# Kernel optimization log

Measured on AMD Instinct MI355X. Metric: run time of the kernel, lower is better.

## Reference

```python
import jax, jax.numpy as jnp
import numpy as np
import math

EMBED_DIM = 64
NUM_HEADS = 4
HEAD_DIM = EMBED_DIM // NUM_HEADS
TGT = 64
SRC = 64
BSZ = 128


def setup_inputs() -> dict:
    key = jax.random.key(0)
    ks = jax.random.split(key, 8)
    x = jax.random.normal(ks[0], (TGT, BSZ, EMBED_DIM), dtype=jnp.float32)
    relation = jax.random.normal(ks[1], (TGT, SRC, BSZ, EMBED_DIM), dtype=jnp.float32)
    in_proj_weight = jax.random.normal(ks[2], (3 * EMBED_DIM, EMBED_DIM), dtype=jnp.float32) * 0.02
    in_proj_bias = jnp.zeros((3 * EMBED_DIM,), dtype=jnp.float32)
    rel_weight = jax.random.normal(ks[3], (2 * EMBED_DIM, EMBED_DIM), dtype=jnp.float32) * 0.02
    rel_bias = jnp.zeros((2 * EMBED_DIM,), dtype=jnp.float32)
    out_weight = jax.random.normal(ks[4], (EMBED_DIM, EMBED_DIM), dtype=jnp.float32) * 0.02
    out_bias = jnp.zeros((EMBED_DIM,), dtype=jnp.float32)
    return {
        'query': x, 'key': x, 'value': x, 'relation': relation,
        'in_proj_weight': in_proj_weight, 'in_proj_bias': in_proj_bias,
        'rel_weight': rel_weight, 'rel_bias': rel_bias,
        'out_weight': out_weight, 'out_bias': out_bias,
    }


def reference(query, key, value, relation, in_proj_weight, in_proj_bias,
              rel_weight, rel_bias, out_weight, out_bias):
    E, H, hd = EMBED_DIM, NUM_HEADS, HEAD_DIM
    t, b, _ = query.shape
    s = key.shape[0]
    scaling = hd ** (-0.5)
    # qkv projections (slices of the fused in_proj weight, as in _in_proj)
    q = query @ in_proj_weight[:E].T + in_proj_bias[:E]
    k = key @ in_proj_weight[E:2 * E].T + in_proj_bias[E:2 * E]
    v = value @ in_proj_weight[2 * E:].T + in_proj_bias[2 * E:]
    q = q.reshape(t, b * H, hd)
    k = k.reshape(s, b * H, hd)
    v = v.reshape(s, b * H, hd)
    # relation projection -> ra, rb, each [t, s, b*H, hd], then transpose(0,1)
    rel = relation @ rel_weight.T + rel_bias  # [t, s, b, 2E]
    ra = rel[..., :E].reshape(t, s, b * H, hd).swapaxes(0, 1)  # [s, t, bH, hd]
    rb = rel[..., E:].reshape(t, s, b * H, hd).swapaxes(0, 1)
    # q[i,j] = q[i] + ra_t[i,j]; requires t == s (broadcast as in torch)
    qp = (q[:, None] + ra) * scaling            # [t, s, bH, hd]
    kp = k[None, :] + rb                        # [t, s, bH, hd]
    attn_weights = jnp.einsum('ijbn,ijbn->ijb', qp, kp) * (1.0 / math.sqrt(hd))
    attn_weights = jax.nn.softmax(attn_weights, axis=1)
    attn = jnp.einsum('ijb,jbn->bin', attn_weights, v)  # [bH, t, hd]
    attn = attn.swapaxes(0, 1).reshape(t, b, E)
    out = attn @ out_weight.T + out_bias
    return out
```

## Files before the change

kernel.cpp:

```cpp
#include <hip/hip_runtime.h>
#include <hip/hip_bf16.h>

#define T_ 64
#define S_ 64
#define B_ 128
#define E_ 64
#define H_ 4

typedef float f32x4 __attribute__((ext_vector_type(4)));
typedef short bf16x8 __attribute__((ext_vector_type(8)));

static __device__ __forceinline__ short f2b(float f) {
    union { __hip_bfloat16 h; short s; } u;
    u.h = __float2bfloat16(f);
    return u.s;
}

__global__ __launch_bounds__(256) void k_qkv(
    const float* __restrict__ qin, const float* __restrict__ kin,
    const float* __restrict__ vin, const float* __restrict__ W,
    const float* __restrict__ bias, float* __restrict__ qkv,
    const float* __restrict__ relW, const float* __restrict__ relBias,
    ushort* __restrict__ wBf, unsigned int* __restrict__ kpbW)
{
    const int tid = threadIdx.x;

    if (blockIdx.x == 256) {
        #pragma unroll
        for (int li = 0; li < 8; ++li) {
            int f4 = li * 256 + tid;
            int o = f4 >> 4, e4 = f4 & 15;
            float4 wv = reinterpret_cast<const float4*>(relW)[f4];
            ushort4 bv;
            bv.x = (ushort)f2b(wv.x); bv.y = (ushort)f2b(wv.y);
            bv.z = (ushort)f2b(wv.z); bv.w = (ushort)f2b(wv.w);
            int ot = o >> 4, cc = o & 15;
            int ks = e4 >> 3, rqb = (e4 & 7) >> 1, half = e4 & 1;
            int dest = (ot * 2 + ks) * 512 + (rqb * 16 + cc) * 8 + half * 4;
            *reinterpret_cast<ushort4*>(wBf + dest) = bv;
        }
        #pragma unroll
        for (int li = 0; li < 8; ++li) {
            int t = li * 256 + tid;
            int ot = t >> 9, lane = (t >> 3) & 63, e = t & 7;
            int cI = lane & 15, rqI = lane >> 4;
            wBf[8192 + t] =
                (rqI * 8 + e == (ot & 1) * 16 + cI) ? (ushort)0x3F80 : (ushort)0;
        }
        return;
    }

    __shared__ float xs[3][32 * 68];
    __shared__ float WTs[64 * 68];
    const int row0 = blockIdx.x * 32;

    #pragma unroll
    for (int l = 0; l < 6; ++l) {
        int f4 = l * 256 + tid;
        int src = f4 >> 9, rem = f4 & 511;
        int r = rem >> 4, e0 = (rem & 15) << 2;
        const float* xin = (src == 0) ? qin : (src == 1 ? kin : vin);
        float4 xv = reinterpret_cast<const float4*>(xin)[(size_t)(row0 + r) * 16 + (e0 >> 2)];
        float* dst = &xs[src][r * 68];
        dst[e0] = xv.x; dst[e0 + 1] = xv.y; dst[e0 + 2] = xv.z; dst[e0 + 3] = xv.w;
    }

    const int rq = tid >> 5, og = tid & 31;
    const int r0 = rq * 4, op0 = og * 2;

    for (int seg = 0; seg < 3; ++seg) {
        __syncthreads();
        #pragma unroll
        for (int l = 0; l < 4; ++l) {
            int f4 = l * 256 + tid;
            int o = f4 >> 4, e0 = (f4 & 15) << 2;
            float4 wv = reinterpret_cast<const float4*>(W)[(size_t)(seg * 64 + o) * 16 + (e0 >> 2)];
            WTs[(e0 + 0) * 68 + o] = wv.x; WTs[(e0 + 1) * 68 + o] = wv.y;
            WTs[(e0 + 2) * 68 + o] = wv.z; WTs[(e0 + 3) * 68 + o] = wv.w;
        }
        __syncthreads();

        float acc[4][2];
        #pragma unroll
        for (int rr = 0; rr < 4; ++rr) {
            acc[rr][0] = bias[seg * 64 + op0];
            acc[rr][1] = bias[seg * 64 + op0 + 1];
        }
        const float* xsrc = xs[seg];
        #pragma unroll 4
        for (int e = 0; e < 64; ++e) {
            float w0 = WTs[e * 68 + op0];
            float w1 = WTs[e * 68 + op0 + 1];
            #pragma unroll
            for (int rr = 0; rr < 4; ++rr) {
                float xv = xsrc[(r0 + rr) * 68 + e];
                acc[rr][0] += xv * w0;
                acc[rr][1] += xv * w1;
            }
        }
        #pragma unroll
        for (int rr = 0; rr < 4; ++rr) {
            float2 ov = make_float2(acc[rr][0], acc[rr][1]);
            reinterpret_cast<float2*>(
                &qkv[((size_t)seg * T_ * B_ + row0 + r0 + rr) * E_ + op0])[0] = ov;
        }
        if (seg == 1) {
            #pragma unroll
            for (int rr = 0; rr < 4; ++rr) {
                int row = row0 + r0 + rr;
                int jj = row >> 7, b = row & 127;
                float kb0 = acc[rr][0] + relBias[64 + op0];
                float kb1 = acc[rr][1] + relBias[64 + op0 + 1];
                unsigned int u = (unsigned int)(ushort)f2b(kb0) |
                                 ((unsigned int)(ushort)f2b(kb1) << 16);
                int off = jj * 8192 + (op0 >> 5) * 4096 + (b >> 4) * 512 +
                          ((b & 15) + ((op0 & 31) >> 3) * 16) * 8 + (op0 & 7);
                kpbW[off >> 1] = u;
            }
        }
    }
}

__global__ __launch_bounds__(512, 4) void k_logits_mfma(
    const float* __restrict__ rel, const ushort* __restrict__ wBf,
    const ushort* __restrict__ kpbF, const float* __restrict__ relBias,
    const float* __restrict__ qkv, float* __restrict__ logits)
{
    __shared__ char  Bs[20480];
    __shared__ float llds[8][64][9];

    const int tid = threadIdx.x;
    const int w = tid >> 6, l = tid & 63;
    const int c = l & 15, rq = l >> 4;
    const int i = blockIdx.x >> 3;
    const int jb = (blockIdx.x & 7) * 8;

    #pragma unroll
    for (int li = 0; li < 3; ++li) {
        int idx = li * 512 + tid;
        if (idx < 1280)
            reinterpret_cast<float4*>(Bs)[idx] =
                reinterpret_cast<const float4*>(wBf)[idx];
    }

    float qpre[4][4];
    {
        const float* qrow = qkv + (size_t)i * (B_ * E_);
        #pragma unroll
        for (int h = 0; h < 4; ++h) {
            float ba = relBias[h * 16 + c];
            #pragma unroll
            for (int r = 0; r < 4; ++r)
                qpre[h][r] = qrow[(w * 16 + rq * 4 + r) * E_ + h * 16 + c] + ba;
        }
    }
    __syncthreads();

    const int arow = (w * 16 + c) * E_ + rq * 8;
    const int kfo  = w * 512 + l * 8;

    float4 x0, x1, x2, x3;
    {
        const float* ab = rel + ((size_t)jb * S_ + i) * (size_t)(B_ * E_) + arow;
        x0 = *(const float4*)(ab);
        x1 = *(const float4*)(ab + 4);
        x2 = *(const float4*)(ab + 32);
        x3 = *(const float4*)(ab + 36);
    }

    #pragma unroll 1
    for (int t = 0; t < 8; ++t) {
        const int j = jb + t;

        bf16x8 kf0 = *(const bf16x8*)(kpbF + (size_t)j * 8192 + kfo);
        bf16x8 kf1 = *(const bf16x8*)(kpbF + (size_t)j * 8192 + 4096 + kfo);

        bf16x8 af0, af1;
        {
            bf16x8 a;
            a[0] = f2b(x0.x); a[1] = f2b(x0.y); a[2] = f2b(x0.z); a[3] = f2b(x0.w);
            a[4] = f2b(x1.x); a[5] = f2b(x1.y); a[6] = f2b(x1.z); a[7] = f2b(x1.w);
            af0 = a;
            a[0] = f2b(x2.x); a[1] = f2b(x2.y); a[2] = f2b(x2.z); a[3] = f2b(x2.w);
            a[4] = f2b(x3.x); a[5] = f2b(x3.y); a[6] = f2b(x3.z); a[7] = f2b(x3.w);
            af1 = a;
        }

        if (t < 7) {
            const float* ab = rel + ((size_t)(j + 1) * S_ + i) * (size_t)(B_ * E_) + arow;
            x0 = *(const float4*)(ab);
            x1 = *(const float4*)(ab + 4);
            x2 = *(const float4*)(ab + 32);
            x3 = *(const float4*)(ab + 36);
        }

        int bs0 = 0;
        asm volatile("" : "+v"(bs0));
        const char* bsp = Bs + bs0;

        f32x4 acc[8];
        #pragma unroll
        for (int ot = 0; ot < 8; ++ot) acc[ot] = (f32x4){0.f, 0.f, 0.f, 0.f};
        #pragma unroll
        for (int ot = 0; ot < 4; ++ot) {
            acc[ot] = __builtin_amdgcn_mfma_f32_16x16x32_bf16(
                af0, *(const bf16x8*)(bsp + (ot * 2 + 0) * 1024 + l * 16), acc[ot], 0, 0, 0);
            acc[ot] = __builtin_amdgcn_mfma_f32_16x16x32_bf16(
                af1, *(const bf16x8*)(bsp + (ot * 2 + 1) * 1024 + l * 16), acc[ot], 0, 0, 0);
        }
        #pragma unroll
        for (int ot = 0; ot < 4; ++ot) {
            acc[4 + ot] = __builtin_amdgcn_mfma_f32_16x16x32_bf16(
                af0, *(const bf16x8*)(bsp + (8 + ot * 2 + 0) * 1024 + l * 16), acc[4 + ot], 0, 0, 0);
            acc[4 + ot] = __builtin_amdgcn_mfma_f32_16x16x32_bf16(
                af1, *(const bf16x8*)(bsp + (8 + ot * 2 + 1) * 1024 + l * 16), acc[4 + ot], 0, 0, 0);
            acc[4 + ot] = __builtin_amdgcn_mfma_f32_16x16x32_bf16(
                (ot < 2 ? kf0 : kf1),
                *(const bf16x8*)(bsp + (16 + ot) * 1024 + l * 16), acc[4 + ot], 0, 0, 0);
        }

        float v[16];
        #pragma unroll
        for (int h = 0; h < 4; ++h)
            #pragma unroll
            for (int r = 0; r < 4; ++r)
                v[h * 4 + r] = (qpre[h][r] + acc[h][r]) * acc[4 + h][r];
        #pragma unroll
        for (int k = 0; k < 8; ++k) {
            float x = (c & 1) ? v[2 * k + 1] : v[2 * k];
            float y = (c & 1) ? v[2 * k] : v[2 * k + 1];
            v[k] = x + __shfl_xor(y, 1);
        }
        #pragma unroll
        for (int k = 0; k < 4; ++k) {
            float x = (c & 2) ? v[2 * k + 1] : v[2 * k];
            float y = (c & 2) ? v[2 * k] : v[2 * k + 1];
            v[k] = x + __shfl_xor(y, 2);
        }
        #pragma unroll
        for (int k = 0; k < 2; ++k) {
            float x = (c & 4) ? v[2 * k + 1] : v[2 * k];
            float y = (c & 4) ? v[2 * k] : v[2 * k + 1];
            v[k] = x + __shfl_xor(y, 4);
        }
        {
            float x = (c & 8) ? v[1] : v[0];
            float y = (c & 8) ? v[0] : v[1];
            llds[w][l][t] = (x + __shfl_xor(y, 8)) * 0.0625f;
        }
    }

    {
        float f[8];
        #pragma unroll
        for (int t2 = 0; t2 < 8; ++t2) f[t2] = llds[w][l][t2];
        const int hh = c >> 2, rr = c & 3;
        const int b = w * 16 + rq * 4 + rr;
        float* dst = &logits[(((size_t)i * B_ + b) * H_ + hh) * S_ + jb];
        *reinterpret_cast<float4*>(dst) = make_float4(f[0], f[1], f[2], f[3]);
        *reinterpret_cast<float4*>(dst + 4) = make_float4(f[4], f[5], f[6], f[7]);
    }
}

__global__ __launch_bounds__(256) void k_attn(
    const float* __restrict__ logits, const float* __restrict__ qkv,
    const float* __restrict__ Wout, const float* __restrict__ bout,
    float* __restrict__ out)
{
    __shared__ float wsm[4][H_][S_];
    __shared__ float ap[4][68];
    const int tid = threadIdx.x;
    const int i = blockIdx.x >> 5;
    const int bq = blockIdx.x & 31;
    const int w = tid >> 6, l = tid & 63;
    const int b = bq * 4 + w;

    const float* lg = logits + ((size_t)i * B_ + b) * H_ * S_;
    const int h = l >> 4, sub = l & 15;
    float v0 = lg[h * S_ + sub];
    float v1 = lg[h * S_ + sub + 16];
    float v2 = lg[h * S_ + sub + 32];
    float v3 = lg[h * S_ + sub + 48];
    float m = fmaxf(fmaxf(v0, v1), fmaxf(v2, v3));
    #pragma unroll
    for (int d = 1; d < 16; d <<= 1) m = fmaxf(m, __shfl_xor(m, d));
    float e0 = expf(v0 - m), e1 = expf(v1 - m), e2 = expf(v2 - m), e3 = expf(v3 - m);
    float ss = e0 + e1 + e2 + e3;
    #pragma unroll
    for (int d = 1; d < 16; d <<= 1) ss += __shfl_xor(ss, d);
    float inv = 1.0f / ss;
    wsm[w][h][sub] = e0 * inv;
    wsm[w][h][sub + 16] = e1 * inv;
    wsm[w][h][sub + 32] = e2 * inv;
    wsm[w][h][sub + 48] = e3 * inv;
    __syncthreads();

    const float* vbase = qkv + (size_t)2 * T_ * B_ * E_ + (size_t)b * E_;
    const float* wrow = &wsm[w][l >> 4][0];
    float acc = 0.f;
    #pragma unroll 4
    for (int j = 0; j < S_; ++j) acc += wrow[j] * vbase[(size_t)j * B_ * E_ + l];
    ap[w][l] = acc;
    __syncthreads();

    const float* wo = Wout + l * E_;
    const float* apw = ap[w];
    float oacc = bout[l];
    #pragma unroll 4
    for (int e = 0; e < E_; ++e) oacc += apw[e] * wo[e];
    out[((size_t)i * B_ + b) * E_ + l] = oacc;
}

extern "C" void kernel_launch(void* const* d_in, const int* in_sizes, int n_in,
                              void* d_out, int out_size, void* d_ws, size_t ws_size,
                              hipStream_t stream)
{
    const float* qin = (const float*)d_in[0];
    const float* kin = (const float*)d_in[1];
    const float* vin = (const float*)d_in[2];
    const float* rel = (const float*)d_in[3];
    const float* ipw = (const float*)d_in[4];
    const float* ipb = (const float*)d_in[5];
    const float* rw  = (const float*)d_in[6];
    const float* rb  = (const float*)d_in[7];
    const float* ow  = (const float*)d_in[8];
    const float* obias = (const float*)d_in[9];

    float* qkv = (float*)d_ws;
    float* logits = qkv + 3 * T_ * B_ * E_;
    ushort* wBf  = (ushort*)(logits + (size_t)T_ * S_ * B_ * H_);
    ushort* kpbF = wBf + 16384;

    float* out = (float*)d_out;

    k_qkv<<<dim3(257), dim3(256), 0, stream>>>(qin, kin, vin, ipw, ipb, qkv,
                                               rw, rb, wBf, (unsigned int*)kpbF);
    k_logits_mfma<<<dim3(512), dim3(512), 0, stream>>>(rel, wBf, kpbF, rb, qkv, logits);
    k_attn<<<dim3(2048), dim3(256), 0, stream>>>(logits, qkv, ow, obias, out);
}
```

Baseline: 66.39 us.

## Reassign logits blocks per source position, stage K in LDS, fold Q via MFMA

The logits kernel now assigns each block one source index j and eight target rows (one per wave), so the k+rb bias tile for j is staged once in LDS instead of being reloaded from global memory per iteration. The q+ra bias term is precomputed in bf16 by the projection kernel and added through an extra MFMA, replacing the fp32 qpre registers, and the per-block LDS transpose of logits is dropped in favour of direct strided stores. The logits layout changes to [i][j][b*H], so the softmax kernel now transposes it through shared memory. Costs are lower q precision (bf16), extra MFMA work, and scattered 4-byte logits stores.

```diff
diff --git a/kernel.cpp b/kernel.cpp
--- a/kernel.cpp
+++ b/kernel.cpp
@@ -21,7 +21,8 @@
     const float* __restrict__ vin, const float* __restrict__ W,
     const float* __restrict__ bias, float* __restrict__ qkv,
     const float* __restrict__ relW, const float* __restrict__ relBias,
-    ushort* __restrict__ wBf, unsigned int* __restrict__ kpbW)
+    ushort* __restrict__ wBf, unsigned int* __restrict__ kpbW,
+    unsigned int* __restrict__ qpbW)
 {
     const int tid = threadIdx.x;
 
@@ -103,6 +104,20 @@
             float2 ov = make_float2(acc[rr][0], acc[rr][1]);
             reinterpret_cast<float2*>(
                 &qkv[((size_t)seg * T_ * B_ + row0 + r0 + rr) * E_ + op0])[0] = ov;
+        }
+        if (seg == 0) {
+            #pragma unroll
+            for (int rr = 0; rr < 4; ++rr) {
+                int row = row0 + r0 + rr;
+                int ii = row >> 7, b = row & 127;
+                float qb0 = acc[rr][0] + relBias[op0];
+                float qb1 = acc[rr][1] + relBias[op0 + 1];
+                unsigned int u = (unsigned int)(ushort)f2b(qb0) |
+                                 ((unsigned int)(ushort)f2b(qb1) << 16);
+                int off = ii * 8192 + (op0 >> 5) * 4096 + (b >> 4) * 512 +
+                          ((b & 15) + ((op0 & 31) >> 3) * 16) * 8 + (op0 & 7);
+                qpbW[off >> 1] = u;
+            }
         }
         if (seg == 1) {
             #pragma unroll
@@ -123,17 +138,18 @@
 
 __global__ __launch_bounds__(512, 4) void k_logits_mfma(
     const float* __restrict__ rel, const ushort* __restrict__ wBf,
-    const ushort* __restrict__ kpbF, const float* __restrict__ relBias,
-    const float* __restrict__ qkv, float* __restrict__ logits)
+    const ushort* __restrict__ kpbF, const ushort* __restrict__ qpbF,
+    float* __restrict__ logits)
 {
-    __shared__ char  Bs[20480];
-    __shared__ float llds[8][64][9];
+    __shared__ char Bs[20480];
+    __shared__ char Ks[16384];
 
     const int tid = threadIdx.x;
     const int w = tid >> 6, l = tid & 63;
     const int c = l & 15, rq = l >> 4;
-    const int i = blockIdx.x >> 3;
-    const int jb = (blockIdx.x & 7) * 8;
+    const int j = blockIdx.x >> 3;
+    const int iblk = blockIdx.x & 7;
+    const int i = iblk * 8 + w;
 
     #pragma unroll
     for (int li = 0; li < 3; ++li) {
@@ -142,39 +158,35 @@
             reinterpret_cast<float4*>(Bs)[idx] =
                 reinterpret_cast<const float4*>(wBf)[idx];
     }
-
-    float qpre[4][4];
     {
-        const float* qrow = qkv + (size_t)i * (B_ * E_);
-        #pragma unroll
-        for (int h = 0; h < 4; ++h) {
-            float ba = relBias[h * 16 + c];
-            #pragma unroll
-            for (int r = 0; r < 4; ++r)
-                qpre[h][r] = qrow[(w * 16 + rq * 4 + r) * E_ + h * 16 + c] + ba;
-        }
+        const float4* kp4 = reinterpret_cast<const float4*>(kpbF + (size_t)j * 8192);
+        reinterpret_cast<float4*>(Ks)[tid] = kp4[tid];
+        reinterpret_cast<float4*>(Ks)[512 + tid] = kp4[512 + tid];
     }
     __syncthreads();
 
-    const int arow = (w * 16 + c) * E_ + rq * 8;
-    const int kfo  = w * 512 + l * 8;
+    const float* relbase = rel + ((size_t)j * S_ + i) * (size_t)(B_ * E_);
+    const int laneoff = c * E_ + rq * 8;
+    const ushort* qpage = qpbF + (size_t)i * 8192;
+    const int qfo = l * 8;
 
     float4 x0, x1, x2, x3;
     {
-        const float* ab = rel + ((size_t)jb * S_ + i) * (size_t)(B_ * E_) + arow;
+        const float* ab = relbase + laneoff;
         x0 = *(const float4*)(ab);
         x1 = *(const float4*)(ab + 4);
         x2 = *(const float4*)(ab + 32);
         x3 = *(const float4*)(ab + 36);
     }
+    bf16x8 qf0c = *(const bf16x8*)(qpage + qfo);
+    bf16x8 qf1c = *(const bf16x8*)(qpage + 4096 + qfo);
+    bf16x8 qf0n = qf0c, qf1n = qf1c;
+
+    float* lbase = logits + ((size_t)i * S_ + j) * (size_t)(B_ * H_);
+    const int soff = rq * 16 + (c & 3) * 4 + (c >> 2);
 
     #pragma unroll 1
-    for (int t = 0; t < 8; ++t) {
-        const int j = jb + t;
-
-        bf16x8 kf0 = *(const bf16x8*)(kpbF + (size_t)j * 8192 + kfo);
-        bf16x8 kf1 = *(const bf16x8*)(kpbF + (size_t)j * 8192 + 4096 + kfo);
-
+    for (int bt = 0; bt < 8; ++bt) {
         bf16x8 af0, af1;
         {
             bf16x8 a;
@@ -186,13 +198,18 @@
             af1 = a;
         }
 
-        if (t < 7) {
-            const float* ab = rel + ((size_t)(j + 1) * S_ + i) * (size_t)(B_ * E_) + arow;
+        if (bt < 7) {
+            const float* ab = relbase + (bt + 1) * 1024 + laneoff;
             x0 = *(const float4*)(ab);
             x1 = *(const float4*)(ab + 4);
             x2 = *(const float4*)(ab + 32);
             x3 = *(const float4*)(ab + 36);
-        }
+            qf0n = *(const bf16x8*)(qpage + (bt + 1) * 512 + qfo);
+            qf1n = *(const bf16x8*)(qpage + 4096 + (bt + 1) * 512 + qfo);
+        }
+
+        bf16x8 kf0 = *(const bf16x8*)(Ks + bt * 1024 + l * 16);
+        bf16x8 kf1 = *(const bf16x8*)(Ks + 8192 + bt * 1024 + l * 16);
 
         int bs0 = 0;
         asm volatile("" : "+v"(bs0));
@@ -207,6 +224,9 @@
                 af0, *(const bf16x8*)(bsp + (ot * 2 + 0) * 1024 + l * 16), acc[ot], 0, 0, 0);
             acc[ot] = __builtin_amdgcn_mfma_f32_16x16x32_bf16(
                 af1, *(const bf16x8*)(bsp + (ot * 2 + 1) * 1024 + l * 16), acc[ot], 0, 0, 0);
+            acc[ot] = __builtin_amdgcn_mfma_f32_16x16x32_bf16(
+                (ot < 2 ? qf0c : qf1c),
+                *(const bf16x8*)(bsp + (16 + ot) * 1024 + l * 16), acc[ot], 0, 0, 0);
         }
         #pragma unroll
         for (int ot = 0; ot < 4; ++ot) {
@@ -224,7 +244,7 @@
         for (int h = 0; h < 4; ++h)
             #pragma unroll
             for (int r = 0; r < 4; ++r)
-                v[h * 4 + r] = (qpre[h][r] + acc[h][r]) * acc[4 + h][r];
+                v[h * 4 + r] = acc[h][r] * acc[4 + h][r];
         #pragma unroll
         for (int k = 0; k < 8; ++k) {
             float x = (c & 1) ? v[2 * k + 1] : v[2 * k];
@@ -243,22 +263,16 @@
             float y = (c & 4) ? v[2 * k] : v[2 * k + 1];
             v[k] = x + __shfl_xor(y, 4);
         }
+        float outv;
         {
             float x = (c & 8) ? v[1] : v[0];
             float y = (c & 8) ? v[0] : v[1];
-            llds[w][l][t] = (x + __shfl_xor(y, 8)) * 0.0625f;
-        }
-    }
-
-    {
-        float f[8];
-        #pragma unroll
-        for (int t2 = 0; t2 < 8; ++t2) f[t2] = llds[w][l][t2];
-        const int hh = c >> 2, rr = c & 3;
-        const int b = w * 16 + rq * 4 + rr;
-        float* dst = &logits[(((size_t)i * B_ + b) * H_ + hh) * S_ + jb];
-        *reinterpret_cast<float4*>(dst) = make_float4(f[0], f[1], f[2], f[3]);
-        *reinterpret_cast<float4*>(dst + 4) = make_float4(f[4], f[5], f[6], f[7]);
+            outv = (x + __shfl_xor(y, 8)) * 0.0625f;
+        }
+
+        lbase[bt * 64 + soff] = outv;
+
+        qf0c = qf0n; qf1c = qf1n;
     }
 }
 
@@ -267,6 +281,7 @@
     const float* __restrict__ Wout, const float* __restrict__ bout,
     float* __restrict__ out)
 {
+    __shared__ float trans[64][20];
     __shared__ float wsm[4][H_][S_];
     __shared__ float ap[4][68];
     const int tid = threadIdx.x;
@@ -275,12 +290,19 @@
     const int w = tid >> 6, l = tid & 63;
     const int b = bq * 4 + w;
 
-    const float* lg = logits + ((size_t)i * B_ + b) * H_ * S_;
+    {
+        const int jj = tid >> 2, q = tid & 3;
+        float4 lv = *(const float4*)(logits + ((size_t)i * S_ + jj) * (B_ * H_) + bq * 16 + q * 4);
+        *reinterpret_cast<float4*>(&trans[jj][q * 4]) = lv;
+    }
+    __syncthreads();
+
     const int h = l >> 4, sub = l & 15;
-    float v0 = lg[h * S_ + sub];
-    float v1 = lg[h * S_ + sub + 16];
-    float v2 = lg[h * S_ + sub + 32];
-    float v3 = lg[h * S_ + sub + 48];
+    const int col = w * 4 + h;
+    float v0 = trans[sub][col];
+    float v1 = trans[sub + 16][col];
+    float v2 = trans[sub + 32][col];
+    float v3 = trans[sub + 48][col];
     float m = fmaxf(fmaxf(v0, v1), fmaxf(v2, v3));
     #pragma unroll
     for (int d = 1; d < 16; d <<= 1) m = fmaxf(m, __shfl_xor(m, d));
@@ -330,11 +352,13 @@
     float* logits = qkv + 3 * T_ * B_ * E_;
     ushort* wBf  = (ushort*)(logits + (size_t)T_ * S_ * B_ * H_);
     ushort* kpbF = wBf + 16384;
+    ushort* qpbF = kpbF + 524288;
 
     float* out = (float*)d_out;
 
     k_qkv<<<dim3(257), dim3(256), 0, stream>>>(qin, kin, vin, ipw, ipb, qkv,
-                                               rw, rb, wBf, (unsigned int*)kpbF);
-    k_logits_mfma<<<dim3(512), dim3(512), 0, stream>>>(rel, wBf, kpbF, rb, qkv, logits);
+                                               rw, rb, wBf, (unsigned int*)kpbF,
+                                               (unsigned int*)qpbF);
+    k_logits_mfma<<<dim3(512), dim3(512), 0, stream>>>(rel, wBf, kpbF, qpbF, logits);
     k_attn<<<dim3(2048), dim3(256), 0, stream>>>(logits, qkv, ow, obias, out);
 }
```

New measurement: 70.27 us. 5.9% more time.
